# Optimization experiments

Measured on AMD Instinct MI355X. Metric: run time of the kernel, lower is better.

Reference implementation:

```python
import jax, jax.numpy as jnp
import numpy as np

N_NODES = 100000
N_EDGES = 1600000
F_IN = 128
HEADS = 4
C_OUT = 32
NEG_SLOPE = 0.2


def setup_inputs() -> dict:
    key = jax.random.key(0)
    k1, k2, k3, k4, k5, k6 = jax.random.split(key, 6)
    x = jax.random.normal(k1, (N_NODES, F_IN), dtype=jnp.float32)
    edge_index = jax.random.randint(k2, (2, N_EDGES), 0, N_NODES, dtype=jnp.int64)
    # glorot-ish scales
    W = jax.random.normal(k3, (F_IN, HEADS * C_OUT), dtype=jnp.float32) * (1.0 / np.sqrt(F_IN))
    att_src = jax.random.normal(k4, (HEADS, C_OUT), dtype=jnp.float32) * (1.0 / np.sqrt(C_OUT))
    att_dst = jax.random.normal(k5, (HEADS, C_OUT), dtype=jnp.float32) * (1.0 / np.sqrt(C_OUT))
    bias = jnp.zeros((HEADS * C_OUT,), dtype=jnp.float32)
    return {"x": x, "edge_index": edge_index, "W": W,
            "att_src": att_src, "att_dst": att_dst, "bias": bias}


def _gat_forward(x, edge_index, W, att_src, att_dst, bias):
    N = x.shape[0]
    H, C = att_src.shape
    h = (x @ W).reshape(N, H, C)                      # [N,H,C]
    # PyG GATConv default: add self-loops
    loops = jnp.arange(N, dtype=edge_index.dtype)
    src = jnp.concatenate([edge_index[0], loops])     # [E+N]
    dst = jnp.concatenate([edge_index[1], loops])
    a_src = jnp.einsum("nhc,hc->nh", h, att_src)      # [N,H]
    a_dst = jnp.einsum("nhc,hc->nh", h, att_dst)
    e = jax.nn.leaky_relu(a_src[src] + a_dst[dst], NEG_SLOPE)  # [E+N,H]
    # segment softmax over destination node (every node has a self-loop)
    m = jax.ops.segment_max(e, dst, num_segments=N)
    e = jnp.exp(e - m[dst])
    s = jax.ops.segment_sum(e, dst, num_segments=N)
    alpha = e / (s[dst] + 1e-16)                      # [E+N,H]
    msg = h[src] * alpha[:, :, None]                  # [E+N,H,C]
    out = jax.ops.segment_sum(msg, dst, num_segments=N).reshape(N, H * C)
    return jnp.tanh(out + bias)


def reference(x, edge_index, W, att_src, att_dst, bias):
    return _gat_forward(x, edge_index, W, att_src, att_dst, bias)
```

## Files before the change

kernel.cpp:

```cpp
#include <hip/hip_runtime.h>
#include <math.h>

#define NN 100000
#define NE 1600000
#define F_IN 128
#define HEADS 4
#define HC 128
#define NEG_SLOPE 0.2f
#define NBKT 391
#define BCAP 5120
#define LDK 136
#define NSTRIP 6250

typedef __attribute__((ext_vector_type(8))) short bf16x8;
typedef __attribute__((ext_vector_type(4))) float f32x4;
typedef __attribute__((ext_vector_type(2))) float f32x2;

static __device__ __forceinline__ short f2bf_rne(float f) {
    unsigned u = __float_as_uint(f);
    unsigned r = (u + 0x7FFFu + ((u >> 16) & 1u)) >> 16;
    return (short)r;
}
static __device__ __forceinline__ float bf2f(short s) {
    return __uint_as_float(((unsigned)(unsigned short)s) << 16);
}
static __device__ __forceinline__ unsigned cvt_pk_bf16(float a, float b) {
    unsigned r;
    asm("v_cvt_pk_bf16_f32 %0, %1, %2" : "=v"(r) : "v"(a), "v"(b));
    return r;
}

static __device__ __forceinline__ void pk_fma(f32x2& d, f32x2 a, f32x2 b) {
    asm("v_pk_fma_f32 %0, %1, %2, %0 op_sel:[0,0,0] op_sel_hi:[1,1,1]"
        : "+v"(d) : "v"(a), "v"(b));
}
static __device__ __forceinline__ void pk_add(f32x2& d, f32x2 a) {
    asm("v_pk_add_f32 %0, %1, %0 op_sel:[0,0] op_sel_hi:[1,1]"
        : "+v"(d) : "v"(a));
}
static __device__ __forceinline__ f32x2 mkpair(float a, float b) {
    f32x2 r; r.x = a; r.y = b; return r;
}

__global__ __launch_bounds__(256) void prep_kernel(
        const float* __restrict__ W, short* __restrict__ wt_hi,
        const int* __restrict__ ei, int* __restrict__ flag) {
    if (blockIdx.x == 0 && threadIdx.x < 64) {
        int l = threadIdx.x;
        int v = ei[2 * l + 1];
        for (int off = 1; off < 64; off <<= 1) v |= __shfl_xor(v, off);
        if (l == 0) *flag = (v == 0) ? 1 : 0;
    }
    int i = blockIdx.x * 256 + threadIdx.x;
    if (i >= F_IN * HC) return;
    int k = i >> 7, n = i & 127;
    wt_hi[n * F_IN + k] = f2bf_rne(W[k * HC + n]);
}

__global__ __launch_bounds__(256) void bucket_scatter_kernel(
        const int* __restrict__ ei, const int* __restrict__ flag,
        int* __restrict__ bcur, unsigned* __restrict__ pairs) {
    __shared__ int lhist[NBKT];
    __shared__ int gbase[NBKT];
    int t = threadIdx.x;
    for (int i = t; i < NBKT; i += 256) lhist[i] = 0;
    __syncthreads();
    int is64 = *flag;
    int base = blockIdx.x * 4096;

    unsigned wrd[16];
    int meta[16];
    if (is64) {
#pragma unroll
        for (int it = 0; it < 8; ++it) {
            int e = base + it * 512 + 2 * t;
            if (e < NE) {
                int4 sv = *(const int4*)(ei + 2 * (size_t)e);
                int4 dv = *(const int4*)(ei + 2 * (size_t)NE + 2 * (size_t)e);
                int b0 = dv.x >> 8;
                int r0 = atomicAdd(&lhist[b0], 1);
                wrd[2 * it] = (unsigned)sv.x | ((unsigned)(dv.x & 255) << 17);
                meta[2 * it] = b0 | (r0 << 9);
                int b1 = dv.z >> 8;
                int r1 = atomicAdd(&lhist[b1], 1);
                wrd[2 * it + 1] = (unsigned)sv.z | ((unsigned)(dv.z & 255) << 17);
                meta[2 * it + 1] = b1 | (r1 << 9);
            } else {
                meta[2 * it] = -1;
                meta[2 * it + 1] = -1;
            }
        }
    } else {
#pragma unroll
        for (int it = 0; it < 16; ++it) {
            int e = base + it * 256 + t;
            if (e < NE) {
                int src = ei[e];
                int dst = ei[NE + e];
                int b = dst >> 8;
                int r = atomicAdd(&lhist[b], 1);
                wrd[it] = (unsigned)src | ((unsigned)(dst & 255) << 17);
                meta[it] = b | (r << 9);
            } else {
                meta[it] = -1;
            }
        }
    }
    __syncthreads();
    for (int i = t; i < NBKT; i += 256)
        gbase[i] = lhist[i] ? atomicAdd(&bcur[i], lhist[i]) : 0;
    __syncthreads();
#pragma unroll
    for (int it = 0; it < 16; ++it) {
        if (meta[it] >= 0) {
            int b = meta[it] & 511;
            int r = meta[it] >> 9;
            pairs[(size_t)b * BCAP + gbase[b] + r] = wrd[it];
        }
    }
}

__global__ __launch_bounds__(512) void mfma_gemm_kernel(
        const float* __restrict__ x, const short* __restrict__ wt_hi,
        unsigned short* __restrict__ h_bf) {
    __shared__ short lw[128 * LDK];
    int t = threadIdx.x;

    for (int c = t; c < 2048; c += 512) {
        int n = c >> 4;
        int kk = (c & 15) * 8;
        *(bf16x8*)(lw + n * LDK + kk) = *(const bf16x8*)(wt_hi + n * F_IN + kk);
    }
    __syncthreads();

    int strip = blockIdx.x * 8 + (t >> 6);
    if (strip >= NSTRIP) return;
    int lane = t & 63;
    int l15 = lane & 15;
    int q = lane >> 4;

    f32x4 acc[8];
#pragma unroll
    for (int nt = 0; nt < 8; ++nt) acc[nt] = (f32x4){0.f, 0.f, 0.f, 0.f};

    union BU { bf16x8 v; unsigned u[4]; };
    const float* xp = x + (size_t)(strip * 16 + l15) * F_IN + q * 8;

#pragma unroll
    for (int ki = 0; ki < 4; ++ki) {
        float4 v0 = *(const float4*)(xp + ki * 32);
        float4 v1 = *(const float4*)(xp + ki * 32 + 4);
        float vv[8] = {v0.x, v0.y, v0.z, v0.w, v1.x, v1.y, v1.z, v1.w};
        BU ah, al;
#pragma unroll
        for (int j = 0; j < 4; ++j) {
            float f0 = vv[2 * j], f1 = vv[2 * j + 1];
            unsigned hp = cvt_pk_bf16(f0, f1);
            ah.u[j] = hp;
            float r0 = f0 - __uint_as_float(hp << 16);
            float r1 = f1 - __uint_as_float(hp & 0xFFFF0000u);
            al.u[j] = cvt_pk_bf16(r0, r1);
        }
        int koff = ki * 32 + q * 8;
#pragma unroll
        for (int nt = 0; nt < 8; ++nt) {
            bf16x8 bh = *(const bf16x8*)(lw + (nt * 16 + l15) * LDK + koff);
            acc[nt] = __builtin_amdgcn_mfma_f32_16x16x32_bf16(ah.v, bh, acc[nt], 0, 0, 0);
            acc[nt] = __builtin_amdgcn_mfma_f32_16x16x32_bf16(al.v, bh, acc[nt], 0, 0, 0);
        }
    }

    int orow = strip * 16 + q * 4;
#pragma unroll
    for (int nt = 0; nt < 8; ++nt)
#pragma unroll
        for (int r = 0; r < 4; ++r)
            h_bf[(size_t)(orow + r) * HC + nt * 16 + l15] =
                (unsigned short)f2bf_rne(acc[nt][r]);
}

__global__ __launch_bounds__(256) void attdot_kernel(
        const unsigned* __restrict__ h2, const float* __restrict__ att_src,
        const float* __restrict__ att_dst,
        float* __restrict__ a_src, float* __restrict__ a_dst) {
    int row = (blockIdx.x * 256 + threadIdx.x) >> 6;
    if (row >= NN) return;
    int lane = threadIdx.x & 63;
    int hd = lane >> 4;
    int l15 = lane & 15;
    unsigned u = h2[(size_t)row * 64 + lane];
    float f0 = __uint_as_float(u << 16);
    float f1 = __uint_as_float(u & 0xFFFF0000u);
    float as0 = att_src[hd * 32 + 2 * l15];
    float as1 = att_src[hd * 32 + 2 * l15 + 1];
    float ad0 = att_dst[hd * 32 + 2 * l15];
    float ad1 = att_dst[hd * 32 + 2 * l15 + 1];
    float ps = f0 * as0 + f1 * as1;
    float pd = f0 * ad0 + f1 * ad1;
#pragma unroll
    for (int off = 1; off < 16; off <<= 1) {
        ps += __shfl_xor(ps, off);
        pd += __shfl_xor(pd, off);
    }
    if (l15 == 0) {
        a_src[row * 4 + hd] = ps;
        a_dst[row * 4 + hd] = pd;
    }
}

__global__ __launch_bounds__(1024) void bucket_csr_kernel(
        const int* __restrict__ bcur, const unsigned* __restrict__ pairs,
        const float* __restrict__ a_src, const float* __restrict__ a_dst,
        int* __restrict__ deg, int* __restrict__ offsets,
        int* __restrict__ csr_src, unsigned* __restrict__ wal) {
    __shared__ unsigned lpairs[BCAP];
    __shared__ int sd[1024];
    __shared__ int cnt256[256];
    __shared__ int lcur[256];

    int b = blockIdx.x;
    int t = threadIdx.x;

    int partial = 0;
    for (int i = t; i < b; i += 1024) partial += bcur[i];
    sd[t] = partial;
    __syncthreads();
    for (int off = 512; off > 0; off >>= 1) {
        if (t < off) sd[t] += sd[t + off];
        __syncthreads();
    }
    int bktbase = sd[0];
    __syncthreads();

    if (t < 256) cnt256[t] = 0;
    __syncthreads();

    int cnt = bcur[b];
    const unsigned* __restrict__ bp = pairs + (size_t)b * BCAP;
    for (int i = t; i < cnt; i += 1024) {
        unsigned w = bp[i];
        lpairs[i] = w;
        atomicAdd(&cnt256[w >> 17], 1);
    }
    __syncthreads();

    if (t < 256) sd[t] = cnt256[t];
    __syncthreads();
    for (int off = 1; off < 256; off <<= 1) {
        int u = 0;
        if (t < 256 && t >= off) u = sd[t - off];
        __syncthreads();
        if (t < 256) sd[t] += u;
        __syncthreads();
    }
    if (t < 256) {
        int v = cnt256[t];
        int myoff = bktbase + sd[t] - v;
        int node = (b << 8) + t;
        if (node < NN) {
            deg[node] = v;
            offsets[node] = myoff;
        }
        lcur[t] = myoff;
    }
    __syncthreads();

#define CSR_EMIT(w_, as_, ad_)                                                  \
    {                                                                           \
        int src_ = (int)(w_ & 0x1FFFFu);                                        \
        int dl_ = (int)(w_ >> 17);                                              \
        float e0 = as_.x + ad_.x; e0 = (e0 < 0.f) ? NEG_SLOPE * e0 : e0;        \
        float e1 = as_.y + ad_.y; e1 = (e1 < 0.f) ? NEG_SLOPE * e1 : e1;        \
        float e2 = as_.z + ad_.z; e2 = (e2 < 0.f) ? NEG_SLOPE * e2 : e2;        \
        float e3 = as_.w + ad_.w; e3 = (e3 < 0.f) ? NEG_SLOPE * e3 : e3;        \
        float w0 = __expf(e0), w1 = __expf(e1), w2 = __expf(e2), w3 = __expf(e3); \
        int pos = atomicAdd(&lcur[dl_], 1);                                     \
        csr_src[pos] = src_;                                                    \
        unsigned lo = (unsigned)(unsigned short)f2bf_rne(w0) |                  \
                      ((unsigned)(unsigned short)f2bf_rne(w1) << 16);           \
        unsigned hi = (unsigned)(unsigned short)f2bf_rne(w2) |                  \
                      ((unsigned)(unsigned short)f2bf_rne(w3) << 16);           \
        ((uint2*)wal)[pos] = make_uint2(lo, hi);                                \
    }

    {
        int i1 = t + 1024, i2 = t + 2048, i3 = t + 3072;
        int v0 = (t < cnt), v1 = (i1 < cnt), v2 = (i2 < cnt), v3 = (i3 < cnt);
        unsigned w0 = 0, w1 = 0, w2 = 0, w3 = 0;
        if (v0) w0 = lpairs[t];
        if (v1) w1 = lpairs[i1];
        if (v2) w2 = lpairs[i2];
        if (v3) w3 = lpairs[i3];
        float4 as0, ad0, as1, ad1, as2, ad2, as3, ad3;
        if (v0) { as0 = ((const float4*)a_src)[w0 & 0x1FFFFu]; ad0 = ((const float4*)a_dst)[(b << 8) + (w0 >> 17)]; }
        if (v1) { as1 = ((const float4*)a_src)[w1 & 0x1FFFFu]; ad1 = ((const float4*)a_dst)[(b << 8) + (w1 >> 17)]; }
        if (v2) { as2 = ((const float4*)a_src)[w2 & 0x1FFFFu]; ad2 = ((const float4*)a_dst)[(b << 8) + (w2 >> 17)]; }
        if (v3) { as3 = ((const float4*)a_src)[w3 & 0x1FFFFu]; ad3 = ((const float4*)a_dst)[(b << 8) + (w3 >> 17)]; }
        if (v0) CSR_EMIT(w0, as0, ad0);
        if (v1) CSR_EMIT(w1, as1, ad1);
        if (v2) CSR_EMIT(w2, as2, ad2);
        if (v3) CSR_EMIT(w3, as3, ad3);
        for (int i = t + 4096; i < cnt; i += 1024) {
            unsigned w = lpairs[i];
            float4 as = ((const float4*)a_src)[w & 0x1FFFFu];
            float4 ad = ((const float4*)a_dst)[(b << 8) + (w >> 17)];
            CSR_EMIT(w, as, ad);
        }
    }
#undef CSR_EMIT
}

__global__ __launch_bounds__(256) void gat_aggr_kernel(
        const int* __restrict__ offsets, const int* __restrict__ deg,
        const int* __restrict__ csr_src, const unsigned* __restrict__ wal,
        const float* __restrict__ a_src, const float* __restrict__ a_dst,
        const unsigned* __restrict__ h2, const float* __restrict__ bias,
        float* __restrict__ out) {
    int wid = (blockIdx.x * 256 + threadIdx.x) >> 6;
    int dst = __builtin_amdgcn_readfirstlane(wid);
    if (dst >= NN) return;
    int lane = threadIdx.x & 63;
    int hd = lane >> 4;
    unsigned hsel2 = (unsigned)(hd & 2);
    unsigned shamt = (hd & 1) ? 0u : 16u;

    int start = offsets[dst];
    int n = deg[dst];

    f32x2 accx2 = {0.f, 0.f}, accy2 = {0.f, 0.f}, ws2 = {0.f, 0.f};

    int j = 0;
    for (; j + 7 < n; j += 8) {
        int base = start + j;
        int s0 = csr_src[base + 0];
        int s1 = csr_src[base + 1];
        int s2 = csr_src[base + 2];
        int s3 = csr_src[base + 3];
        int s4 = csr_src[base + 4];
        int s5 = csr_src[base + 5];
        int s6 = csr_src[base + 6];
        int s7 = csr_src[base + 7];
        uint2 wv0 = ((const uint2*)wal)[base + 0];
        uint2 wv1 = ((const uint2*)wal)[base + 1];
        uint2 wv2 = ((const uint2*)wal)[base + 2];
        uint2 wv3 = ((const uint2*)wal)[base + 3];
        uint2 wv4 = ((const uint2*)wal)[base + 4];
        uint2 wv5 = ((const uint2*)wal)[base + 5];
        uint2 wv6 = ((const uint2*)wal)[base + 6];
        uint2 wv7 = ((const uint2*)wal)[base + 7];
        unsigned u0 = h2[(size_t)s0 * 64 + lane];
        unsigned u1 = h2[(size_t)s1 * 64 + lane];
        unsigned u2 = h2[(size_t)s2 * 64 + lane];
        unsigned u3 = h2[(size_t)s3 * 64 + lane];
        unsigned u4 = h2[(size_t)s4 * 64 + lane];
        unsigned u5 = h2[(size_t)s5 * 64 + lane];
        unsigned u6 = h2[(size_t)s6 * 64 + lane];
        unsigned u7 = h2[(size_t)s7 * 64 + lane];
#define EDGEPAIR(ua, ub, wva, wvb)                                              \
        {                                                                       \
            unsigned wsa = hsel2 ? wva.y : wva.x;                               \
            unsigned wsb = hsel2 ? wvb.y : wvb.x;                               \
            f32x2 wp = mkpair(__uint_as_float((wsa << shamt) & 0xFFFF0000u),    \
                              __uint_as_float((wsb << shamt) & 0xFFFF0000u));   \
            f32x2 hx = mkpair(__uint_as_float(ua << 16),                        \
                              __uint_as_float(ub << 16));                       \
            f32x2 hy = mkpair(__uint_as_float(ua & 0xFFFF0000u),                \
                              __uint_as_float(ub & 0xFFFF0000u));               \
            pk_add(ws2, wp);                                                    \
            pk_fma(accx2, wp, hx);                                              \
            pk_fma(accy2, wp, hy);                                              \
        }
        EDGEPAIR(u0, u1, wv0, wv1)
        EDGEPAIR(u2, u3, wv2, wv3)
        EDGEPAIR(u4, u5, wv4, wv5)
        EDGEPAIR(u6, u7, wv6, wv7)
    }
    for (; j + 1 < n; j += 2) {
        int base = start + j;
        int s0 = csr_src[base + 0];
        int s1 = csr_src[base + 1];
        uint2 wv0 = ((const uint2*)wal)[base + 0];
        uint2 wv1 = ((const uint2*)wal)[base + 1];
        unsigned u0 = h2[(size_t)s0 * 64 + lane];
        unsigned u1 = h2[(size_t)s1 * 64 + lane];
        EDGEPAIR(u0, u1, wv0, wv1)
    }
#undef EDGEPAIR
    float accx = accx2.x + accx2.y;
    float accy = accy2.x + accy2.y;
    float wsum = ws2.x + ws2.y;
    if (j < n) {
        int base = start + j;
        int s0 = csr_src[base];
        uint2 wv0 = ((const uint2*)wal)[base];
        unsigned u0 = h2[(size_t)s0 * 64 + lane];
        unsigned ws0 = hsel2 ? wv0.y : wv0.x;
        float w0 = __uint_as_float((ws0 << shamt) & 0xFFFF0000u);
        wsum += w0;
        accx += w0 * __uint_as_float(u0 << 16);
        accy += w0 * __uint_as_float(u0 & 0xFFFF0000u);
    }

    float e = a_src[dst * 4 + hd] + a_dst[dst * 4 + hd];
    e = (e < 0.f) ? NEG_SLOPE * e : e;
    float sf = __expf(e);
    float inv = 1.f / (wsum + sf + 1e-16f);

    unsigned us = h2[(size_t)dst * 64 + lane];
    float2 b2 = ((const float2*)bias)[lane];
    float ox = tanhf((accx + sf * __uint_as_float(us << 16)) * inv + b2.x);
    float oy = tanhf((accy + sf * __uint_as_float(us & 0xFFFF0000u)) * inv + b2.y);
    ((float2*)out)[(size_t)dst * 64 + lane] = make_float2(ox, oy);
}

extern "C" void kernel_launch(void* const* d_in, const int* in_sizes, int n_in,
                              void* d_out, int out_size, void* d_ws, size_t ws_size,
                              hipStream_t stream) {
    const float* x       = (const float*)d_in[0];
    const int*   ei      = (const int*)  d_in[1];
    const float* W       = (const float*)d_in[2];
    const float* att_src = (const float*)d_in[3];
    const float* att_dst = (const float*)d_in[4];
    const float* bias    = (const float*)d_in[5];
    float* out = (float*)d_out;

    unsigned short* h_bf = (unsigned short*)d_ws;
    float* a_src = (float*)(h_bf + (size_t)NN * HC);
    float* a_dst = a_src + (size_t)NN * HEADS;
    short* wt_hi = (short*)(a_dst + (size_t)NN * HEADS);
    int* flag    = (int*)(wt_hi + F_IN * HC);
    int* bcur    = flag + 4;
    int* deg     = bcur + NBKT + 1;
    int* offsets = deg + NN;
    int* csr_src = offsets + NN;
    unsigned* wal = (unsigned*)(csr_src + NE);
    unsigned* pairs = (unsigned*)(wal + (size_t)NE * 2);

    hipMemsetAsync(bcur, 0, NBKT * sizeof(int), stream);

    hipLaunchKernelGGL(prep_kernel, dim3(64), dim3(256), 0, stream,
                       W, wt_hi, ei, flag);

    hipLaunchKernelGGL(bucket_scatter_kernel, dim3((NE + 4095) / 4096), dim3(256), 0, stream,
                       ei, flag, bcur, pairs);

    hipLaunchKernelGGL(mfma_gemm_kernel, dim3(782), dim3(512), 0, stream,
                       x, wt_hi, h_bf);

    hipLaunchKernelGGL(attdot_kernel, dim3(NN * 64 / 256), dim3(256), 0, stream,
                       (const unsigned*)h_bf, att_src, att_dst, a_src, a_dst);

    hipLaunchKernelGGL(bucket_csr_kernel, dim3(NBKT), dim3(1024), 0, stream,
                       bcur, pairs, a_src, a_dst, deg, offsets, csr_src, wal);

    hipLaunchKernelGGL(gat_aggr_kernel, dim3(NN * 64 / 256), dim3(256), 0, stream,
                       offsets, deg, csr_src, wal, a_src, a_dst,
                       (const unsigned*)h_bf, bias, out);
}
```

Baseline: 254.0 us.

## Store features and edge weights head-major and aggregate per head slice

The GEMM now writes h in a head-major layout [head][node][32] and the CSR kernel writes the bf16 edge weights as four separate per-head planes. The aggregation kernel is restructured so that each block handles one head for four destination nodes. Each wavefront splits that node's edges across four 16-lane groups and then reduces with shuffles. The aim is to shrink each head's working set so gathers are better cached per head, at the cost of four times as many blocks, re-reading csr_src once per head, and a reduction step at the end.

```diff
diff --git a/kernel.cpp b/kernel.cpp
--- a/kernel.cpp
+++ b/kernel.cpp
@@ -14,32 +14,16 @@
 
 typedef __attribute__((ext_vector_type(8))) short bf16x8;
 typedef __attribute__((ext_vector_type(4))) float f32x4;
-typedef __attribute__((ext_vector_type(2))) float f32x2;
 
 static __device__ __forceinline__ short f2bf_rne(float f) {
     unsigned u = __float_as_uint(f);
     unsigned r = (u + 0x7FFFu + ((u >> 16) & 1u)) >> 16;
     return (short)r;
 }
-static __device__ __forceinline__ float bf2f(short s) {
-    return __uint_as_float(((unsigned)(unsigned short)s) << 16);
-}
 static __device__ __forceinline__ unsigned cvt_pk_bf16(float a, float b) {
     unsigned r;
     asm("v_cvt_pk_bf16_f32 %0, %1, %2" : "=v"(r) : "v"(a), "v"(b));
     return r;
-}
-
-static __device__ __forceinline__ void pk_fma(f32x2& d, f32x2 a, f32x2 b) {
-    asm("v_pk_fma_f32 %0, %1, %2, %0 op_sel:[0,0,0] op_sel_hi:[1,1,1]"
-        : "+v"(d) : "v"(a), "v"(b));
-}
-static __device__ __forceinline__ void pk_add(f32x2& d, f32x2 a) {
-    asm("v_pk_add_f32 %0, %1, %0 op_sel:[0,0] op_sel_hi:[1,1]"
-        : "+v"(d) : "v"(a));
-}
-static __device__ __forceinline__ f32x2 mkpair(float a, float b) {
-    f32x2 r; r.x = a; r.y = b; return r;
 }
 
 __global__ __launch_bounds__(256) void prep_kernel(
@@ -122,7 +106,7 @@
 
 __global__ __launch_bounds__(512) void mfma_gemm_kernel(
         const float* __restrict__ x, const short* __restrict__ wt_hi,
-        unsigned short* __restrict__ h_bf) {
+        unsigned short* __restrict__ hq) {
     __shared__ short lw[128 * LDK];
     int t = threadIdx.x;
 
@@ -172,15 +156,18 @@
 
     int orow = strip * 16 + q * 4;
 #pragma unroll
-    for (int nt = 0; nt < 8; ++nt)
+    for (int nt = 0; nt < 8; ++nt) {
+        int hd = nt >> 1;
+        int colh = (nt & 1) * 16 + l15;
 #pragma unroll
         for (int r = 0; r < 4; ++r)
-            h_bf[(size_t)(orow + r) * HC + nt * 16 + l15] =
+            hq[(size_t)hd * NN * 32 + (size_t)(orow + r) * 32 + colh] =
                 (unsigned short)f2bf_rne(acc[nt][r]);
+    }
 }
 
 __global__ __launch_bounds__(256) void attdot_kernel(
-        const unsigned* __restrict__ h2, const float* __restrict__ att_src,
+        const unsigned* __restrict__ hq_u, const float* __restrict__ att_src,
         const float* __restrict__ att_dst,
         float* __restrict__ a_src, float* __restrict__ a_dst) {
     int row = (blockIdx.x * 256 + threadIdx.x) >> 6;
@@ -188,7 +175,7 @@
     int lane = threadIdx.x & 63;
     int hd = lane >> 4;
     int l15 = lane & 15;
-    unsigned u = h2[(size_t)row * 64 + lane];
+    unsigned u = hq_u[(size_t)hd * NN * 16 + (size_t)row * 16 + l15];
     float f0 = __uint_as_float(u << 16);
     float f1 = __uint_as_float(u & 0xFFFF0000u);
     float as0 = att_src[hd * 32 + 2 * l15];
@@ -212,7 +199,7 @@
         const int* __restrict__ bcur, const unsigned* __restrict__ pairs,
         const float* __restrict__ a_src, const float* __restrict__ a_dst,
         int* __restrict__ deg, int* __restrict__ offsets,
-        int* __restrict__ csr_src, unsigned* __restrict__ wal) {
+        int* __restrict__ csr_src, unsigned short* __restrict__ walh) {
     __shared__ unsigned lpairs[BCAP];
     __shared__ int sd[1024];
     __shared__ int cnt256[256];
@@ -276,11 +263,10 @@
         float w0 = __expf(e0), w1 = __expf(e1), w2 = __expf(e2), w3 = __expf(e3); \
         int pos = atomicAdd(&lcur[dl_], 1);                                     \
         csr_src[pos] = src_;                                                    \
-        unsigned lo = (unsigned)(unsigned short)f2bf_rne(w0) |                  \
-                      ((unsigned)(unsigned short)f2bf_rne(w1) << 16);           \
-        unsigned hi = (unsigned)(unsigned short)f2bf_rne(w2) |                  \
-                      ((unsigned)(unsigned short)f2bf_rne(w3) << 16);           \
-        ((uint2*)wal)[pos] = make_uint2(lo, hi);                                \
+        walh[pos]                      = (unsigned short)f2bf_rne(w0);          \
+        walh[(size_t)NE + pos]         = (unsigned short)f2bf_rne(w1);          \
+        walh[(size_t)2 * NE + pos]     = (unsigned short)f2bf_rne(w2);          \
+        walh[(size_t)3 * NE + pos]     = (unsigned short)f2bf_rne(w3);          \
     }
 
     {
@@ -312,105 +298,66 @@
 
 __global__ __launch_bounds__(256) void gat_aggr_kernel(
         const int* __restrict__ offsets, const int* __restrict__ deg,
-        const int* __restrict__ csr_src, const unsigned* __restrict__ wal,
+        const int* __restrict__ csr_src, const unsigned short* __restrict__ walh,
         const float* __restrict__ a_src, const float* __restrict__ a_dst,
-        const unsigned* __restrict__ h2, const float* __restrict__ bias,
+        const unsigned* __restrict__ hq_u, const float* __restrict__ bias,
         float* __restrict__ out) {
-    int wid = (blockIdx.x * 256 + threadIdx.x) >> 6;
-    int dst = __builtin_amdgcn_readfirstlane(wid);
-    if (dst >= NN) return;
+    int b = blockIdx.x;
+    int q = b & 3;
+    int dst = (b >> 2) * 4 + (threadIdx.x >> 6);
     int lane = threadIdx.x & 63;
-    int hd = lane >> 4;
-    unsigned hsel2 = (unsigned)(hd & 2);
-    unsigned shamt = (hd & 1) ? 0u : 16u;
+    int sub = lane >> 4;
+    int l15 = lane & 15;
 
     int start = offsets[dst];
     int n = deg[dst];
-
-    f32x2 accx2 = {0.f, 0.f}, accy2 = {0.f, 0.f}, ws2 = {0.f, 0.f};
-
+    const unsigned* __restrict__ hqq = hq_u + (size_t)q * NN * 16;
+    const unsigned short* __restrict__ wq = walh + (size_t)q * NE;
+
+    float accx = 0.f, accy = 0.f, wsum = 0.f;
     int j = 0;
     for (; j + 7 < n; j += 8) {
-        int base = start + j;
-        int s0 = csr_src[base + 0];
-        int s1 = csr_src[base + 1];
-        int s2 = csr_src[base + 2];
-        int s3 = csr_src[base + 3];
-        int s4 = csr_src[base + 4];
-        int s5 = csr_src[base + 5];
-        int s6 = csr_src[base + 6];
-        int s7 = csr_src[base + 7];
-        uint2 wv0 = ((const uint2*)wal)[base + 0];
-        uint2 wv1 = ((const uint2*)wal)[base + 1];
-        uint2 wv2 = ((const uint2*)wal)[base + 2];
-        uint2 wv3 = ((const uint2*)wal)[base + 3];
-        uint2 wv4 = ((const uint2*)wal)[base + 4];
-        uint2 wv5 = ((const uint2*)wal)[base + 5];
-        uint2 wv6 = ((const uint2*)wal)[base + 6];
-        uint2 wv7 = ((const uint2*)wal)[base + 7];
-        unsigned u0 = h2[(size_t)s0 * 64 + lane];
-        unsigned u1 = h2[(size_t)s1 * 64 + lane];
-        unsigned u2 = h2[(size_t)s2 * 64 + lane];
-        unsigned u3 = h2[(size_t)s3 * 64 + lane];
-        unsigned u4 = h2[(size_t)s4 * 64 + lane];
-        unsigned u5 = h2[(size_t)s5 * 64 + lane];
-        unsigned u6 = h2[(size_t)s6 * 64 + lane];
-        unsigned u7 = h2[(size_t)s7 * 64 + lane];
-#define EDGEPAIR(ua, ub, wva, wvb)                                              \
-        {                                                                       \
-            unsigned wsa = hsel2 ? wva.y : wva.x;                               \
-            unsigned wsb = hsel2 ? wvb.y : wvb.x;                               \
-            f32x2 wp = mkpair(__uint_as_float((wsa << shamt) & 0xFFFF0000u),    \
-                              __uint_as_float((wsb << shamt) & 0xFFFF0000u));   \
-            f32x2 hx = mkpair(__uint_as_float(ua << 16),                        \
-                              __uint_as_float(ub << 16));                       \
-            f32x2 hy = mkpair(__uint_as_float(ua & 0xFFFF0000u),                \
-                              __uint_as_float(ub & 0xFFFF0000u));               \
-            pk_add(ws2, wp);                                                    \
-            pk_fma(accx2, wp, hx);                                              \
-            pk_fma(accy2, wp, hy);                                              \
-        }
-        EDGEPAIR(u0, u1, wv0, wv1)
-        EDGEPAIR(u2, u3, wv2, wv3)
-        EDGEPAIR(u4, u5, wv4, wv5)
-        EDGEPAIR(u6, u7, wv6, wv7)
-    }
-    for (; j + 1 < n; j += 2) {
-        int base = start + j;
-        int s0 = csr_src[base + 0];
-        int s1 = csr_src[base + 1];
-        uint2 wv0 = ((const uint2*)wal)[base + 0];
-        uint2 wv1 = ((const uint2*)wal)[base + 1];
-        unsigned u0 = h2[(size_t)s0 * 64 + lane];
-        unsigned u1 = h2[(size_t)s1 * 64 + lane];
-        EDGEPAIR(u0, u1, wv0, wv1)
-    }
-#undef EDGEPAIR
-    float accx = accx2.x + accx2.y;
-    float accy = accy2.x + accy2.y;
-    float wsum = ws2.x + ws2.y;
-    if (j < n) {
-        int base = start + j;
-        int s0 = csr_src[base];
-        uint2 wv0 = ((const uint2*)wal)[base];
-        unsigned u0 = h2[(size_t)s0 * 64 + lane];
-        unsigned ws0 = hsel2 ? wv0.y : wv0.x;
-        float w0 = __uint_as_float((ws0 << shamt) & 0xFFFF0000u);
-        wsum += w0;
+        int e0 = start + j + sub;
+        int e1 = e0 + 4;
+        int s0 = csr_src[e0];
+        int s1 = csr_src[e1];
+        float w0 = __uint_as_float((unsigned)wq[e0] << 16);
+        float w1 = __uint_as_float((unsigned)wq[e1] << 16);
+        unsigned u0 = hqq[(size_t)s0 * 16 + l15];
+        unsigned u1 = hqq[(size_t)s1 * 16 + l15];
+        wsum += w0 + w1;
         accx += w0 * __uint_as_float(u0 << 16);
         accy += w0 * __uint_as_float(u0 & 0xFFFF0000u);
-    }
-
-    float e = a_src[dst * 4 + hd] + a_dst[dst * 4 + hd];
-    e = (e < 0.f) ? NEG_SLOPE * e : e;
-    float sf = __expf(e);
-    float inv = 1.f / (wsum + sf + 1e-16f);
-
-    unsigned us = h2[(size_t)dst * 64 + lane];
-    float2 b2 = ((const float2*)bias)[lane];
-    float ox = tanhf((accx + sf * __uint_as_float(us << 16)) * inv + b2.x);
-    float oy = tanhf((accy + sf * __uint_as_float(us & 0xFFFF0000u)) * inv + b2.y);
-    ((float2*)out)[(size_t)dst * 64 + lane] = make_float2(ox, oy);
+        accx += w1 * __uint_as_float(u1 << 16);
+        accy += w1 * __uint_as_float(u1 & 0xFFFF0000u);
+    }
+    for (; j < n; j += 4) {
+        int idx = j + sub;
+        if (idx < n) {
+            int e0 = start + idx;
+            int s0 = csr_src[e0];
+            float w0 = __uint_as_float((unsigned)wq[e0] << 16);
+            unsigned u0 = hqq[(size_t)s0 * 16 + l15];
+            wsum += w0;
+            accx += w0 * __uint_as_float(u0 << 16);
+            accy += w0 * __uint_as_float(u0 & 0xFFFF0000u);
+        }
+    }
+    accx += __shfl_xor(accx, 16); accx += __shfl_xor(accx, 32);
+    accy += __shfl_xor(accy, 16); accy += __shfl_xor(accy, 32);
+    wsum += __shfl_xor(wsum, 16); wsum += __shfl_xor(wsum, 32);
+
+    if (sub == 0) {
+        float e = a_src[dst * 4 + q] + a_dst[dst * 4 + q];
+        e = (e < 0.f) ? NEG_SLOPE * e : e;
+        float sf = __expf(e);
+        float inv = 1.f / (wsum + sf + 1e-16f);
+        unsigned us = hqq[(size_t)dst * 16 + l15];
+        float2 b2 = ((const float2*)bias)[q * 16 + l15];
+        float ox = tanhf((accx + sf * __uint_as_float(us << 16)) * inv + b2.x);
+        float oy = tanhf((accy + sf * __uint_as_float(us & 0xFFFF0000u)) * inv + b2.y);
+        ((float2*)out)[(size_t)dst * 64 + q * 16 + l15] = make_float2(ox, oy);
+    }
 }
 
 extern "C" void kernel_launch(void* const* d_in, const int* in_sizes, int n_in,
@@ -424,8 +371,8 @@
     const float* bias    = (const float*)d_in[5];
     float* out = (float*)d_out;
 
-    unsigned short* h_bf = (unsigned short*)d_ws;
-    float* a_src = (float*)(h_bf + (size_t)NN * HC);
+    unsigned short* hq = (unsigned short*)d_ws;
+    float* a_src = (float*)(hq + (size_t)NN * HC);
     float* a_dst = a_src + (size_t)NN * HEADS;
     short* wt_hi = (short*)(a_dst + (size_t)NN * HEADS);
     int* flag    = (int*)(wt_hi + F_IN * HC);
@@ -433,8 +380,8 @@
     int* deg     = bcur + NBKT + 1;
     int* offsets = deg + NN;
     int* csr_src = offsets + NN;
-    unsigned* wal = (unsigned*)(csr_src + NE);
-    unsigned* pairs = (unsigned*)(wal + (size_t)NE * 2);
+    unsigned short* walh = (unsigned short*)(csr_src + NE);
+    unsigned* pairs = (unsigned*)(walh + (size_t)4 * NE);
 
     hipMemsetAsync(bcur, 0, NBKT * sizeof(int), stream);
 
@@ -445,15 +392,15 @@
                        ei, flag, bcur, pairs);
 
     hipLaunchKernelGGL(mfma_gemm_kernel, dim3(782), dim3(512), 0, stream,
-                       x, wt_hi, h_bf);
+                       x, wt_hi, hq);
 
     hipLaunchKernelGGL(attdot_kernel, dim3(NN * 64 / 256), dim3(256), 0, stream,
-                       (const unsigned*)h_bf, att_src, att_dst, a_src, a_dst);
+                       (const unsigned*)hq, att_src, att_dst, a_src, a_dst);
 
     hipLaunchKernelGGL(bucket_csr_kernel, dim3(NBKT), dim3(1024), 0, stream,
-                       bcur, pairs, a_src, a_dst, deg, offsets, csr_src, wal);
-
-    hipLaunchKernelGGL(gat_aggr_kernel, dim3(NN * 64 / 256), dim3(256), 0, stream,
-                       offsets, deg, csr_src, wal, a_src, a_dst,
-                       (const unsigned*)h_bf, bias, out);
-}
+                       bcur, pairs, a_src, a_dst, deg, offsets, csr_src, walh);
+
+    hipLaunchKernelGGL(gat_aggr_kernel, dim3(NN), dim3(256), 0, stream,
+                       offsets, deg, csr_src, walh, a_src, a_dst,
+                       (const unsigned*)hq, bias, out);
+}
```

New measurement: 377.8 us. +48.7%, slower.
